# Optimization experiments

Hardware: AMD Instinct MI355X
Metric: run time of the kernel (lower is better)

## Reference

```python
import jax, jax.numpy as jnp
import numpy as np

BS, NS, NSTEP = 128, 1024, 8
IN_DIM, HID, MLP = 768, 512, 512
NEG = -100000.0


def setup_inputs() -> dict:
    key = jax.random.key(0)
    ks = jax.random.split(key, 12)
    s_h = 1.0 / np.sqrt(HID)
    s_cat = 1.0 / np.sqrt(HID + IN_DIM)
    s_m = 1.0 / np.sqrt(MLP)
    # gumbel noise implements Categorical sampling as argmax(logits + gumbel)
    u = jax.random.uniform(ks[9], (NSTEP, BS, NS), jnp.float32, 1e-7, 1.0 - 1e-7)
    return {
        "target_emb": jax.random.normal(ks[0], (BS, IN_DIM), jnp.float32),
        "ctx_emb": jax.random.normal(ks[1], (BS, NS, IN_DIM), jnp.float32),
        "target_len": jax.random.randint(ks[2], (BS,), 1, 32),
        "ctx_len": jax.random.randint(ks[3], (BS,), NSTEP, NS + 1),
        "n_step": NSTEP,
        "W_ih": jax.random.normal(ks[4], (4 * HID, IN_DIM), jnp.float32) * s_h,
        "W_hh": jax.random.normal(ks[5], (4 * HID, HID), jnp.float32) * s_h,
        "b_ih": jnp.zeros((4 * HID,), jnp.float32),
        "b_hh": jnp.zeros((4 * HID,), jnp.float32),
        "W1c": jax.random.normal(ks[6], (MLP, IN_DIM), jnp.float32) * s_cat,
        "W1h": jax.random.normal(ks[7], (MLP, HID), jnp.float32) * s_cat,
        "b1": jnp.zeros((MLP,), jnp.float32),
        "w2": jax.random.normal(ks[8], (MLP,), jnp.float32) * s_m,
        "b2": jnp.zeros((), jnp.float32),
        "gumbel": -jnp.log(-jnp.log(u)),
    }


def reference(target_emb, ctx_emb, target_len, ctx_len, n_step,
              W_ih, W_hh, b_ih, b_hh, W1c, W1h, b1, w2, b2, gumbel):
    bs, ns, in_dim = ctx_emb.shape
    hid = W_hh.shape[1]
    # mlp1 split: ctx part is constant across steps (concat([ctx, h]) @ W1^T = ctx@W1c^T + h@W1h^T)
    ctx_part = jnp.einsum('bnd,md->bnm', ctx_emb, W1c) + b1  # [bs, ns, mlp]
    mask0 = jnp.where(jnp.arange(ns)[None, :] >= ctx_len[:, None], NEG, 0.0).astype(jnp.float32)
    h0 = jnp.zeros((bs, hid), jnp.float32)
    c0 = jnp.zeros((bs, hid), jnp.float32)
    lp0 = jnp.zeros((bs,), jnp.float32)
    batch_idx = jnp.arange(bs)

    def step(carry, g):
        h, c, mask, x, lp = carry
        # LSTMCell (torch gate order: i, f, g, o); dropout is identity (eval semantics)
        gates = x @ W_ih.T + b_ih + h @ W_hh.T + b_hh
        i_g, f_g, g_g, o_g = jnp.split(gates, 4, axis=-1)
        c_new = jax.nn.sigmoid(f_g) * c + jax.nn.sigmoid(i_g) * jnp.tanh(g_g)
        h_new = jax.nn.sigmoid(o_g) * jnp.tanh(c_new)
        # attention-style MLP score
        pre = ctx_part + (h_new @ W1h.T)[:, None, :]          # [bs, ns, mlp]
        sc = jnp.tanh(pre) @ w2 + b2 + mask                   # [bs, ns]
        # Categorical(probs=softmax(sc)).sample() via Gumbel-argmax
        out = jnp.argmax(sc + g, axis=-1)                     # [bs]
        lp = lp + jnp.take_along_axis(jax.nn.log_softmax(sc, axis=-1), out[:, None], 1)[:, 0]
        mask = mask.at[batch_idx, out].set(NEG)
        x_new = jnp.take_along_axis(ctx_emb, out[:, None, None], axis=1)[:, 0, :]
        return (h_new, c_new, mask, x_new, lp), out

    (h, c, mask, x, log_probs), outputs = jax.lax.scan(
        step, (h0, c0, mask0, target_emb, lp0), gumbel)
    return outputs, log_probs
```

## Files before the change

### kernel.cpp

```cpp
#include <hip/hip_runtime.h>
#include <hip/hip_bf16.h>

#define BSZ 128
#define NSQ 1024
#define NSTEPC 8
#define IND 768
#define HIDD 512
#define G4D 2048
#define MLPD 512
#define KXD 1280
#define NEGV -100000.0f
#define KSG 16
#define KSH 8
#define MSPLIT 4

typedef __attribute__((ext_vector_type(4))) float f32x4;
typedef __attribute__((ext_vector_type(8))) short short8v;

__device__ __forceinline__ void split2(float4 f0, float4 f1, short8v& hi, short8v& lo) {
  float fv[8] = {f0.x, f0.y, f0.z, f0.w, f1.x, f1.y, f1.z, f1.w};
#pragma unroll
  for (int j = 0; j < 8; ++j) {
    const unsigned ub = __builtin_bit_cast(unsigned, fv[j]);
    const unsigned hb = ub & 0xFFFF0000u;
    const float lf = fv[j] - __builtin_bit_cast(float, hb);
    hi[j] = (short)(hb >> 16);
    lo[j] = (short)(__builtin_bit_cast(unsigned, lf) >> 16);
  }
}

__device__ __forceinline__ float tanh_fast(float x) {
  x = fminf(fmaxf(x, -15.0f), 15.0f);
  float e = __builtin_amdgcn_exp2f(x * 2.8853900817779268f);
  float r = __builtin_amdgcn_rcpf(e + 1.0f);
  return fmaf(-2.0f, r, 1.0f);
}

__global__ __launch_bounds__(256) void k_prep_wfrag(
    const float* __restrict__ W1c,
    unsigned short* __restrict__ wfh, unsigned short* __restrict__ wfl) {
  const int c = blockIdx.x * 256 + threadIdx.x;
  if (c >= 49152) return;
  const int row = c / 96, wc = c - row * 96;
  const int mxwm = row >> 6;
  const int f = (row >> 4) & 3, l15 = row & 15;
  const int t = wc >> 2, l4 = wc & 3;
  const size_t unit = (((size_t)(mxwm * 24 + t) * 4 + f) * 64) + l4 * 16 + l15;
  const float* src = W1c + (size_t)row * IND + wc * 8;
  const float4 f0 = *(const float4*)src, f1 = *(const float4*)(src + 4);
  short8v hi, lo;
  split2(f0, f1, hi, lo);
  *(short8v*)(wfh + unit * 8) = hi;
  *(short8v*)(wfl + unit * 8) = lo;
}

__global__ __launch_bounds__(256) void k_init(
    const float* __restrict__ te, const int* __restrict__ cl,
    float* __restrict__ mask, float* __restrict__ xh,
    float* __restrict__ cst, float* __restrict__ lp) {
  const int b = blockIdx.x, tid = threadIdx.x;
  const int L = cl[b];
  for (int n = tid; n < NSQ; n += 256) mask[(size_t)b*NSQ + n] = (n >= L) ? NEGV : 0.0f;
  for (int d = tid; d < IND; d += 256) xh[(size_t)b*KXD + d] = te[(size_t)b*IND + d];
  for (int j = tid; j < HIDD; j += 256) {
    xh[(size_t)b*KXD + IND + j] = 0.0f;
    cst[(size_t)b*HIDD + j] = 0.0f;
  }
  if (tid == 0) lp[b] = 0.0f;
}

struct TileRegs {
  short8v wh[4], wl[4];
  float4 ca[4], cb[4];
};

__device__ __forceinline__ void ld_tile(
    TileRegs& T, const unsigned short* __restrict__ wfh,
    const unsigned short* __restrict__ wfl, size_t wbase,
    const float* __restrict__ cbase, int t) {
  const size_t toff = wbase + (size_t)t * 2048;
#pragma unroll
  for (int f = 0; f < 4; ++f) {
    T.wh[f] = *(const short8v*)(wfh + toff + f * 512);
    T.wl[f] = *(const short8v*)(wfl + toff + f * 512);
    const float* s = cbase + (size_t)(f * 16) * IND + t * 32;
    T.ca[f] = *(const float4*)s;
    T.cb[f] = *(const float4*)(s + 4);
  }
}

__device__ __forceinline__ void do_tile(TileRegs& T, f32x4 acc[4][4]) {
  short8v bh[4], bl[4];
#pragma unroll
  for (int f = 0; f < 4; ++f) split2(T.ca[f], T.cb[f], bh[f], bl[f]);
  __builtin_amdgcn_s_setprio(1);
#pragma unroll
  for (int fm = 0; fm < 4; ++fm)
#pragma unroll
    for (int fn = 0; fn < 4; ++fn) {
      acc[fm][fn] = __builtin_amdgcn_mfma_f32_16x16x32_bf16(T.wh[fm], bh[fn], acc[fm][fn], 0, 0, 0);
      acc[fm][fn] = __builtin_amdgcn_mfma_f32_16x16x32_bf16(T.wh[fm], bl[fn], acc[fm][fn], 0, 0, 0);
      acc[fm][fn] = __builtin_amdgcn_mfma_f32_16x16x32_bf16(T.wl[fm], bh[fn], acc[fm][fn], 0, 0, 0);
    }
  __builtin_amdgcn_s_setprio(0);
}

__global__ __launch_bounds__(256, 2) void k_ctx8(
    const float* __restrict__ ctx,
    const unsigned short* __restrict__ wfh, const unsigned short* __restrict__ wfl,
    const float* __restrict__ bias, const int* __restrict__ clen,
    float* __restrict__ cp) {
  const int bid = blockIdx.x;
  const int v = ((bid & 7) << 9) + (bid >> 3);
  const int mx = v & 3;
  const int rbC = v >> 2;
  const int b = rbC >> 3;
  const int nbase = (rbC & 7) << 7;
  if (nbase >= clen[b]) return;
  const int i0 = rbC << 7;
  const int m0 = mx << 7;
  const int tid = threadIdx.x;
  const int lane = tid & 63, wid = tid >> 6;
  const int wm = wid & 1, wn = wid >> 1;
  const int l15 = lane & 15, l4 = lane >> 4;

  const size_t wbase = (size_t)((mx * 2 + wm) * 24) * 2048 + lane * 8;
  const float* cbase = ctx + (size_t)(i0 + wn * 64 + l15) * IND + l4 * 8;

  f32x4 acc[4][4] = {};
  TileRegs A, B;
  ld_tile(A, wfh, wfl, wbase, cbase, 0);
  for (int t = 0; t < 24; t += 2) {
    ld_tile(B, wfh, wfl, wbase, cbase, t + 1);
    do_tile(A, acc);
    if (t + 2 < 24) ld_tile(A, wfh, wfl, wbase, cbase, t + 2);
    do_tile(B, acc);
  }
#pragma unroll
  for (int fm = 0; fm < 4; ++fm) {
#pragma unroll
    for (int r = 0; r < 4; ++r) {
      const int m = m0 + wm * 64 + fm * 16 + l4 * 4 + r;
      const float bb = bias[m];
      float* dst = cp + (((size_t)(b * MLPD + m)) << 10) + nbase + wn * 64 + l15;
#pragma unroll
      for (int fn = 0; fn < 4; ++fn)
        dst[fn * 16] = acc[fm][fn][r] + bb;
    }
  }
}

__global__ __launch_bounds__(256) void k_pgemm(
    const float* __restrict__ A, int lda, int acol,
    const float* __restrict__ B0, int ldb0, int kb,
    const float* __restrict__ B1, int ldb1,
    int kTiles, int N, float* __restrict__ P) {
  __shared__ float As[16][128];
  __shared__ float Bs[16][132];
  const int n0 = blockIdx.x * 128;
  const int kc0 = blockIdx.y * kTiles * 16;
  const int tid = threadIdx.x;
  const int tn = tid & 15;
  const int ta = tid >> 4;
  float acc[8][8] = {};
  for (int t = 0; t < kTiles; ++t) {
    const int k0 = kc0 + t * 16;
#pragma unroll
    for (int u = 0; u < 2; ++u) {
      const int v = tid + u * 256;
      const int r = v >> 2, kc = v & 3;
      const float4 a4 = *(const float4*)(A + (size_t)r * lda + acol + k0 + kc * 4);
      As[kc*4+0][r] = a4.x; As[kc*4+1][r] = a4.y; As[kc*4+2][r] = a4.z; As[kc*4+3][r] = a4.w;
      const float* bp = (k0 < kb) ? (B0 + (size_t)(n0 + r) * ldb0 + k0 + kc * 4)
                                  : (B1 + (size_t)(n0 + r) * ldb1 + (k0 - kb) + kc * 4);
      const float4 b4 = *(const float4*)bp;
      Bs[kc*4+0][r] = b4.x; Bs[kc*4+1][r] = b4.y; Bs[kc*4+2][r] = b4.z; Bs[kc*4+3][r] = b4.w;
    }
    __syncthreads();
#pragma unroll
    for (int kk = 0; kk < 16; ++kk) {
      float av[8], bv[8];
#pragma unroll
      for (int q = 0; q < 8; ++q) av[q] = As[kk][ta*8+q];
#pragma unroll
      for (int q = 0; q < 8; ++q) bv[q] = Bs[kk][tn*8+q];
#pragma unroll
      for (int ri = 0; ri < 8; ++ri)
#pragma unroll
        for (int ni = 0; ni < 8; ++ni)
          acc[ri][ni] = fmaf(av[ri], bv[ni], acc[ri][ni]);
    }
    __syncthreads();
  }
#pragma unroll
  for (int ri = 0; ri < 8; ++ri) {
    const int i = ta * 8 + ri;
    float* p = P + ((size_t)blockIdx.y * BSZ + i) * N + n0 + tn * 8;
    *(float4*)(p + 0) = make_float4(acc[ri][0], acc[ri][1], acc[ri][2], acc[ri][3]);
    *(float4*)(p + 4) = make_float4(acc[ri][4], acc[ri][5], acc[ri][6], acc[ri][7]);
  }
}

__global__ __launch_bounds__(512) void k_lstm(
    const float* __restrict__ gp, const float* __restrict__ b_ih,
    const float* __restrict__ b_hh, float* __restrict__ cst, float* __restrict__ xh) {
  const int b = blockIdx.x, j = threadIdx.x;
  float g[4];
#pragma unroll
  for (int q = 0; q < 4; ++q) {
    float s = b_ih[q*HIDD + j] + b_hh[q*HIDD + j];
#pragma unroll
    for (int ks = 0; ks < KSG; ++ks) s += gp[((size_t)ks*BSZ + b)*G4D + q*HIDD + j];
    g[q] = s;
  }
  const float c_old = cst[(size_t)b*HIDD + j];
  const float ig = 1.0f / (1.0f + expf(-g[0]));
  const float fg = 1.0f / (1.0f + expf(-g[1]));
  const float gg = tanhf(g[2]);
  const float og = 1.0f / (1.0f + expf(-g[3]));
  const float cn = fg * c_old + ig * gg;
  const float hn = og * tanhf(cn);
  cst[(size_t)b*HIDD + j] = cn;
  xh[(size_t)b*KXD + IND + j] = hn;
}

__global__ __launch_bounds__(256) void k_scores(
    const float* __restrict__ cp, const float* __restrict__ hpp,
    const float* __restrict__ w2, const int* __restrict__ clen,
    float* __restrict__ psc) {
  const int mh = blockIdx.x;
  const int b = blockIdx.y;
  const int tid = threadIdx.x;
  __shared__ float hs[128], ws[128];
  if (tid < 128) {
    const int m = mh * 128 + tid;
    float s = 0.0f;
#pragma unroll
    for (int ks = 0; ks < KSH; ++ks) s += hpp[((size_t)ks*BSZ + b)*MLPD + m];
    hs[tid] = s;
    ws[tid] = w2[m];
  }
  __syncthreads();
  const int len = clen[b];
  const int n0 = tid * 4;
  if (n0 >= len) return;
  float ax = 0, ay = 0, az = 0, aw = 0;
  const float* base = cp + ((size_t)b * MLPD + mh * 128) * NSQ + n0;
#pragma unroll 4
  for (int mm = 0; mm < 128; ++mm) {
    const float4 c4 = *(const float4*)(base + (size_t)mm * NSQ);
    const float h = hs[mm], w = ws[mm];
    ax = fmaf(tanh_fast(c4.x + h), w, ax);
    ay = fmaf(tanh_fast(c4.y + h), w, ay);
    az = fmaf(tanh_fast(c4.z + h), w, az);
    aw = fmaf(tanh_fast(c4.w + h), w, aw);
  }
  *(float4*)(psc + ((size_t)b * MSPLIT + mh) * NSQ + n0) = make_float4(ax, ay, az, aw);
}

__global__ __launch_bounds__(256) void k_argmax(
    const float* __restrict__ psc, float* __restrict__ mask,
    const float* __restrict__ gum, const float* __restrict__ b2p,
    float* __restrict__ lp, const float* __restrict__ ctx,
    float* __restrict__ xh, float* __restrict__ outv, int step) {
  const int b = blockIdx.x, tid = threadIdx.x;
  __shared__ float rv[256], rs[256], rm[256];
  __shared__ int ri[256];
  __shared__ int sel;
  const float b2 = b2p[0];
  const int n0 = tid * 4;
  const float4 m4 = *(const float4*)(mask + (size_t)b * NSQ + n0);
  float sc[4] = {b2 + m4.x, b2 + m4.y, b2 + m4.z, b2 + m4.w};
#pragma unroll
  for (int mh = 0; mh < MSPLIT; ++mh) {
    const float4 p4 = *(const float4*)(psc + ((size_t)b * MSPLIT + mh) * NSQ + n0);
    sc[0] += p4.x; sc[1] += p4.y; sc[2] += p4.z; sc[3] += p4.w;
  }
  const float4 g4 = *(const float4*)(gum + ((size_t)step * BSZ + b) * NSQ + n0);
  const float gv[4] = {g4.x, g4.y, g4.z, g4.w};
  float bestv = -1e30f, bests = 0.0f, msc = -1e30f;
  int bestn = 0;
#pragma unroll
  for (int q = 0; q < 4; ++q) {
    const float v = sc[q] + gv[q];
    if (v > bestv) { bestv = v; bestn = n0 + q; bests = sc[q]; }
    msc = fmaxf(msc, sc[q]);
  }
  rv[tid] = bestv; ri[tid] = bestn; rs[tid] = bests; rm[tid] = msc;
  __syncthreads();
  for (int o = 128; o > 0; o >>= 1) {
    if (tid < o) {
      if (rv[tid+o] > rv[tid] || (rv[tid+o] == rv[tid] && ri[tid+o] < ri[tid])) {
        rv[tid] = rv[tid+o]; ri[tid] = ri[tid+o]; rs[tid] = rs[tid+o];
      }
      rm[tid] = fmaxf(rm[tid], rm[tid+o]);
    }
    __syncthreads();
  }
  const float M = rm[0];
  __syncthreads();
  float se = 0.0f;
#pragma unroll
  for (int q = 0; q < 4; ++q)
    se += __builtin_amdgcn_exp2f((sc[q] - M) * 1.4426950408889634f);
  rm[tid] = se;
  __syncthreads();
  for (int o = 128; o > 0; o >>= 1) {
    if (tid < o) rm[tid] += rm[tid+o];
    __syncthreads();
  }
  if (tid == 0) {
    const int n = ri[0];
    const float lse = M + logf(rm[0]);
    const float nlp = lp[b] + rs[0] - lse;
    lp[b] = nlp;
    mask[(size_t)b * NSQ + n] = NEGV;
    outv[step * BSZ + b] = (float)n;
    if (step == NSTEPC - 1) outv[NSTEPC * BSZ + b] = nlp;
    sel = n;
  }
  __syncthreads();
  const int n = sel;
  const float4* src = (const float4*)(ctx + ((size_t)b * NSQ + n) * IND);
  float4* dst = (float4*)(xh + (size_t)b * KXD);
  for (int d = tid; d < IND / 4; d += 256) dst[d] = src[d];
}

extern "C" void kernel_launch(void* const* d_in, const int* in_sizes, int n_in,
                              void* d_out, int out_size, void* d_ws, size_t ws_size,
                              hipStream_t stream) {
  const float* target_emb = (const float*)d_in[0];
  const float* ctx_emb   = (const float*)d_in[1];
  const int*   ctx_len   = (const int*)d_in[3];
  const float* W_ih = (const float*)d_in[5];
  const float* W_hh = (const float*)d_in[6];
  const float* b_ih = (const float*)d_in[7];
  const float* b_hh = (const float*)d_in[8];
  const float* W1c  = (const float*)d_in[9];
  const float* W1h  = (const float*)d_in[10];
  const float* b1   = (const float*)d_in[11];
  const float* w2   = (const float*)d_in[12];
  const float* b2   = (const float*)d_in[13];
  const float* gumbel = (const float*)d_in[14];
  float* out = (float*)d_out;

  float* ws = (float*)d_ws;
  size_t off = 0;
  auto alloc = [&](size_t n) { float* p = ws + off; off += (n + 63) & ~(size_t)63; return p; };

  float* cp   = alloc((size_t)BSZ * MLPD * NSQ);
  float* gp   = alloc((size_t)KSG * BSZ * G4D);
  float* hpp  = alloc((size_t)KSH * BSZ * MLPD);
  float* psc  = alloc((size_t)BSZ * MSPLIT * NSQ);
  float* mask = alloc((size_t)BSZ * NSQ);
  float* xh   = alloc((size_t)BSZ * KXD);
  float* cst  = alloc((size_t)BSZ * HIDD);
  float* lp   = alloc(128);
  unsigned short* wfh = (unsigned short*)alloc(196608);
  unsigned short* wfl = (unsigned short*)alloc(196608);

  k_prep_wfrag<<<192, 256, 0, stream>>>(W1c, wfh, wfl);
  k_init<<<BSZ, 256, 0, stream>>>(target_emb, ctx_len, mask, xh, cst, lp);
  k_ctx8<<<4096, 256, 0, stream>>>(ctx_emb, wfh, wfl, b1, ctx_len, cp);

  for (int t = 0; t < NSTEPC; ++t) {
    k_pgemm<<<dim3(G4D/128, KSG), 256, 0, stream>>>(
        xh, KXD, 0, W_ih, IND, IND, W_hh, HIDD, 5, G4D, gp);
    k_lstm<<<BSZ, 512, 0, stream>>>(gp, b_ih, b_hh, cst, xh);
    k_pgemm<<<dim3(MLPD/128, KSH), 256, 0, stream>>>(
        xh, KXD, IND, W1h, HIDD, 1 << 30, nullptr, 0, 4, MLPD, hpp);
    k_scores<<<dim3(MSPLIT, BSZ), 256, 0, stream>>>(cp, hpp, w2, ctx_len, psc);
    k_argmax<<<BSZ, 256, 0, stream>>>(psc, mask, gumbel, b2, lp, ctx_emb, xh, out, t);
  }
}
```

Measured before the change: 864.3 us.

## Restructure ctx projection GEMM to share split-bf16 context tiles via LDS

The ctx_emb x W1c projection kernel now uses one 512-thread block per 128-row context strip, with each of the 8 waves covering 64 output columns. Previously four blocks each reloaded and re-split the same context rows. The context tile is split into bf16 hi/lo once per k-step and stored in double-buffered, XOR-swizzled shared memory for all waves to read. This removes the 4x redundant global reads and split conversions of ctx_emb. In exchange it adds a __syncthreads per k-step, holds twice as many accumulators per wave, and limits occupancy to one block per CU.

```diff
diff --git a/kernel.cpp b/kernel.cpp
--- a/kernel.cpp
+++ b/kernel.cpp
@@ -42,10 +42,10 @@
   const int c = blockIdx.x * 256 + threadIdx.x;
   if (c >= 49152) return;
   const int row = c / 96, wc = c - row * 96;
-  const int mxwm = row >> 6;
+  const int w = row >> 6;
   const int f = (row >> 4) & 3, l15 = row & 15;
   const int t = wc >> 2, l4 = wc & 3;
-  const size_t unit = (((size_t)(mxwm * 24 + t) * 4 + f) * 64) + l4 * 16 + l15;
+  const size_t unit = (((size_t)(w * 24 + t) * 4 + f) * 64) + l4 * 16 + l15;
   const float* src = W1c + (size_t)row * IND + wc * 8;
   const float4 f0 = *(const float4*)src, f1 = *(const float4*)(src + 4);
   short8v hi, lo;
@@ -69,82 +69,79 @@
   if (tid == 0) lp[b] = 0.0f;
 }
 
-struct TileRegs {
-  short8v wh[4], wl[4];
-  float4 ca[4], cb[4];
-};
-
-__device__ __forceinline__ void ld_tile(
-    TileRegs& T, const unsigned short* __restrict__ wfh,
-    const unsigned short* __restrict__ wfl, size_t wbase,
-    const float* __restrict__ cbase, int t) {
-  const size_t toff = wbase + (size_t)t * 2048;
-#pragma unroll
-  for (int f = 0; f < 4; ++f) {
-    T.wh[f] = *(const short8v*)(wfh + toff + f * 512);
-    T.wl[f] = *(const short8v*)(wfl + toff + f * 512);
-    const float* s = cbase + (size_t)(f * 16) * IND + t * 32;
-    T.ca[f] = *(const float4*)s;
-    T.cb[f] = *(const float4*)(s + 4);
-  }
-}
-
-__device__ __forceinline__ void do_tile(TileRegs& T, f32x4 acc[4][4]) {
-  short8v bh[4], bl[4];
-#pragma unroll
-  for (int f = 0; f < 4; ++f) split2(T.ca[f], T.cb[f], bh[f], bl[f]);
-  __builtin_amdgcn_s_setprio(1);
-#pragma unroll
-  for (int fm = 0; fm < 4; ++fm)
-#pragma unroll
-    for (int fn = 0; fn < 4; ++fn) {
-      acc[fm][fn] = __builtin_amdgcn_mfma_f32_16x16x32_bf16(T.wh[fm], bh[fn], acc[fm][fn], 0, 0, 0);
-      acc[fm][fn] = __builtin_amdgcn_mfma_f32_16x16x32_bf16(T.wh[fm], bl[fn], acc[fm][fn], 0, 0, 0);
-      acc[fm][fn] = __builtin_amdgcn_mfma_f32_16x16x32_bf16(T.wl[fm], bh[fn], acc[fm][fn], 0, 0, 0);
-    }
-  __builtin_amdgcn_s_setprio(0);
-}
-
-__global__ __launch_bounds__(256, 2) void k_ctx8(
+__global__ __launch_bounds__(512, 1) void k_ctx9(
     const float* __restrict__ ctx,
     const unsigned short* __restrict__ wfh, const unsigned short* __restrict__ wfl,
     const float* __restrict__ bias, const int* __restrict__ clen,
     float* __restrict__ cp) {
-  const int bid = blockIdx.x;
-  const int v = ((bid & 7) << 9) + (bid >> 3);
-  const int mx = v & 3;
-  const int rbC = v >> 2;
-  const int b = rbC >> 3;
-  const int nbase = (rbC & 7) << 7;
+  __shared__ __align__(16) unsigned short sCh[2][4096], sCl[2][4096];
+  const int strip = blockIdx.x;
+  const int b = strip >> 3;
+  const int nbase = (strip & 7) << 7;
   if (nbase >= clen[b]) return;
-  const int i0 = rbC << 7;
-  const int m0 = mx << 7;
+  const int i0 = strip << 7;
   const int tid = threadIdx.x;
   const int lane = tid & 63, wid = tid >> 6;
-  const int wm = wid & 1, wn = wid >> 1;
   const int l15 = lane & 15, l4 = lane >> 4;
-
-  const size_t wbase = (size_t)((mx * 2 + wm) * 24) * 2048 + lane * 8;
-  const float* cbase = ctx + (size_t)(i0 + wn * 64 + l15) * IND + l4 * 8;
-
-  f32x4 acc[4][4] = {};
-  TileRegs A, B;
-  ld_tile(A, wfh, wfl, wbase, cbase, 0);
-  for (int t = 0; t < 24; t += 2) {
-    ld_tile(B, wfh, wfl, wbase, cbase, t + 1);
-    do_tile(A, acc);
-    if (t + 2 < 24) ld_tile(A, wfh, wfl, wbase, cbase, t + 2);
-    do_tile(B, acc);
+  const int crow = tid >> 2, cs = tid & 3;
+  const int kread = cs ^ ((crow >> 1) & 3);
+  const float* csrc = ctx + (size_t)(i0 + crow) * IND + kread * 8;
+  const size_t wbase = (size_t)(wid * 24) * 2048 + lane * 8;
+
+  {
+    short8v hi, lo;
+    split2(*(const float4*)csrc, *(const float4*)(csrc + 4), hi, lo);
+    *(short8v*)&sCh[0][tid * 8] = hi;
+    *(short8v*)&sCl[0][tid * 8] = lo;
+  }
+
+  f32x4 acc[4][8] = {};
+  for (int t = 0; t < 24; ++t) {
+    __syncthreads();
+    const int cur = t & 1;
+    float4 q0, q1;
+    if (t + 1 < 24) {
+      q0 = *(const float4*)(csrc + (t + 1) * 32);
+      q1 = *(const float4*)(csrc + (t + 1) * 32 + 4);
+    }
+    short8v wh[4], wl[4];
+    const size_t toff = wbase + (size_t)t * 2048;
+#pragma unroll
+    for (int f = 0; f < 4; ++f) {
+      wh[f] = *(const short8v*)(wfh + toff + f * 512);
+      wl[f] = *(const short8v*)(wfl + toff + f * 512);
+    }
+#pragma unroll
+    for (int fn = 0; fn < 8; ++fn) {
+      const int rc = fn * 16 + l15;
+      const int so = (l4 ^ ((rc >> 1) & 3)) << 3;
+      const short8v bhv = *(const short8v*)&sCh[cur][rc * 32 + so];
+      const short8v blv = *(const short8v*)&sCl[cur][rc * 32 + so];
+      __builtin_amdgcn_s_setprio(1);
+#pragma unroll
+      for (int fm = 0; fm < 4; ++fm) {
+        acc[fm][fn] = __builtin_amdgcn_mfma_f32_16x16x32_bf16(wh[fm], bhv, acc[fm][fn], 0, 0, 0);
+        acc[fm][fn] = __builtin_amdgcn_mfma_f32_16x16x32_bf16(wh[fm], blv, acc[fm][fn], 0, 0, 0);
+        acc[fm][fn] = __builtin_amdgcn_mfma_f32_16x16x32_bf16(wl[fm], bhv, acc[fm][fn], 0, 0, 0);
+      }
+      __builtin_amdgcn_s_setprio(0);
+    }
+    if (t + 1 < 24) {
+      short8v hi, lo;
+      split2(q0, q1, hi, lo);
+      *(short8v*)&sCh[cur ^ 1][tid * 8] = hi;
+      *(short8v*)&sCl[cur ^ 1][tid * 8] = lo;
+    }
   }
 #pragma unroll
   for (int fm = 0; fm < 4; ++fm) {
 #pragma unroll
     for (int r = 0; r < 4; ++r) {
-      const int m = m0 + wm * 64 + fm * 16 + l4 * 4 + r;
+      const int m = wid * 64 + fm * 16 + l4 * 4 + r;
       const float bb = bias[m];
-      float* dst = cp + (((size_t)(b * MLPD + m)) << 10) + nbase + wn * 64 + l15;
-#pragma unroll
-      for (int fn = 0; fn < 4; ++fn)
+      float* dst = cp + (((size_t)(b * MLPD + m)) << 10) + nbase + l15;
+#pragma unroll
+      for (int fn = 0; fn < 8; ++fn)
         dst[fn * 16] = acc[fm][fn][r] + bb;
     }
   }
@@ -361,7 +358,7 @@
 
   k_prep_wfrag<<<192, 256, 0, stream>>>(W1c, wfh, wfl);
   k_init<<<BSZ, 256, 0, stream>>>(target_emb, ctx_len, mask, xh, cst, lp);
-  k_ctx8<<<4096, 256, 0, stream>>>(ctx_emb, wfh, wfl, b1, ctx_len, cp);
+  k_ctx9<<<1024, 512, 0, stream>>>(ctx_emb, wfh, wfl, b1, ctx_len, cp);
 
   for (int t = 0; t < NSTEPC; ++t) {
     k_pgemm<<<dim3(G4D/128, KSG), 256, 0, stream>>>(
```

Measured after the change: 857.0 us. No clear change (-0.8%).
